# Kernel optimization log

Measured on AMD Instinct MI355X. Metric: run time of the kernel, lower is better.

Reference implementation:

```python
import jax, jax.numpy as jnp
import numpy as np

B, S, NODE, DEP, R, L, E = 32, 1024, 256, 64, 50, 16, 128


def setup_inputs() -> dict:
    key = jax.random.key(0)
    k1, k2, k3, k4, k5 = jax.random.split(key, 5)
    context = jax.random.normal(k1, (B, S, NODE), dtype=jnp.float32)
    # torch.rand -> uniform [0,1); one [dep, node+dep] matrix per dependency relation
    dep_W = jax.random.uniform(k2, (R, DEP, NODE + DEP), dtype=jnp.float32)
    heads = jax.random.randint(k3, (B, L, E), 0, S, dtype=jnp.int32)
    tails = jax.random.randint(k4, (B, L, E), 0, S, dtype=jnp.int32)
    rels = jax.random.randint(k5, (B, L, E), 0, R, dtype=jnp.int32)
    return {"context": context, "dep_W": dep_W, "heads": heads, "tails": tails, "rels": rels}


def reference(context, dep_W, heads, tails, rels):
    # context: [B,S,node]; dep_W: [R,dep,node+dep]; heads/tails/rels: [B,L,E]
    B_, S_, node = context.shape
    dep = dep_W.shape[1]
    E_ = heads.shape[2]
    batch_off = jnp.arange(B_, dtype=jnp.int32)[:, None] * S_  # [B,1]

    def layer_step(child, layer):
        h, t, r = layer  # each [B,E]
        # gather per-edge tail features (node feature ++ child state from deeper layers)
        ctx_t = jnp.take_along_axis(context, t[:, :, None], axis=1)  # [B,E,node]
        chd_t = jnp.take_along_axis(child, t[:, :, None], axis=1)    # [B,E,dep]
        feat = jnp.concatenate([ctx_t, chd_t], axis=-1)              # [B,E,node+dep]
        W_e = dep_W[r]                                               # [B,E,dep,node+dep]
        # sum(W * feat, dim=1) == relation-indexed matvec
        msg = jnp.einsum('bekd,bed->bek', W_e, feat)                 # [B,E,dep]
        # scatter-average messages onto head nodes (per batch -> flat index)
        idx = (batch_off + h).reshape(-1)                            # [B*E]
        seg = jax.ops.segment_sum(msg.reshape(-1, dep), idx, num_segments=B_ * S_)
        cnt = jax.ops.segment_sum(jnp.ones((B_ * E_,), msg.dtype), idx, num_segments=B_ * S_)
        avg = seg / jnp.maximum(cnt, 1.0)[:, None]
        child_flat = child.reshape(B_ * S_, dep)
        # heads touched this layer get the averaged message (assignment semantics)
        child_new = jnp.where((cnt > 0)[:, None], avg, child_flat).reshape(B_, S_, dep)
        return child_new, None

    child0 = jnp.zeros((B_, S_, dep), context.dtype)
    layers = (jnp.moveaxis(heads, 1, 0), jnp.moveaxis(tails, 1, 0), jnp.moveaxis(rels, 1, 0))
    child, _ = jax.lax.scan(layer_step, child0, layers)  # layer 0 = deepest layer
    return jnp.concatenate([context, child], axis=-1)    # [B,S,node+dep]
```

## Files before the change

### kernel.cpp

```cpp
#include <hip/hip_runtime.h>

constexpr int B_ = 32;
constexpr int S_ = 1024;
constexpr int NODE_ = 256;
constexpr int DEP_ = 64;
constexpr int R_ = 50;
constexpr int L_ = 16;
constexpr int E_ = 128;
constexpr int FEAT_ = NODE_ + DEP_;
constexpr int NEDGE_ = B_ * E_;
constexpr int BS_ = B_ * S_;
constexpr int CH_ = 16;
constexpr int NCH_ = 320;
constexpr int PREB_ = 512;
constexpr int GCH_ = 64;
constexpr int NGC_ = 1088;

constexpr size_t N_CHILD  = (size_t)BS_ * DEP_;
constexpr size_t OFF_A0   = N_CHILD;
constexpr size_t OFF_WT   = N_CHILD * 4;
constexpr size_t N_WT     = (size_t)R_ * FEAT_ * DEP_;
constexpr size_t OFF_SORT = OFF_WT + N_WT;
constexpr size_t N_SORT   = (size_t)L_ * NEDGE_;
constexpr size_t OFF_CHUNK= OFF_SORT + N_SORT;
constexpr size_t N_CHUNK_I= (size_t)L_ * NCH_ * 4;
constexpr size_t OFF_HC   = OFF_CHUNK + N_CHUNK_I;
constexpr size_t N_HC     = (size_t)L_ * BS_;
constexpr size_t OFF_MT   = OFF_HC + N_HC;
constexpr size_t OFF_MH   = OFF_MT + N_SORT;
constexpr size_t OFF_MI   = OFF_MH + N_SORT;
constexpr size_t OFF_CD   = OFF_MI + N_SORT;
constexpr size_t N_CD     = (size_t)L_ * NEDGE_ * DEP_;
constexpr size_t OFF_GIDX = OFF_CD + N_CD;
constexpr size_t OFF_GCH  = OFF_GIDX + N_SORT;
constexpr size_t OFF_HLR  = OFF_GCH + (size_t)NGC_ * 4;
constexpr size_t OFF_SLR  = OFF_HLR + (size_t)L_ * R_;

__global__ void k_pre(const float* __restrict__ W, const int* __restrict__ rels,
                      const int* __restrict__ heads,
                      float* __restrict__ WT2, int* __restrict__ sorted,
                      int4* __restrict__ chunks, int* __restrict__ hc,
                      float* __restrict__ zero_base,
                      int* __restrict__ hist_lr, int* __restrict__ start_lr) {
  int blk = blockIdx.x, tid = threadIdx.x;
  if (blk < L_) {
    int l = blk;
    __shared__ int hist[R_], startA[R_], rank[R_], cstart[R_];
    __shared__ int ntot;
    if (tid < R_) { hist[tid] = 0; rank[tid] = 0; }
    int* hcl = hc + (size_t)l * BS_;
    for (int i = tid; i < BS_; i += 256) hcl[i] = 0;
    __syncthreads();
    for (int ed = tid; ed < NEDGE_; ed += 256) {
      int b = ed >> 7, e = ed & (E_ - 1);
      atomicAdd(&hist[rels[(b * L_ + l) * E_ + e]], 1);
      atomicAdd(&hcl[b * S_ + heads[(b * L_ + l) * E_ + e]], 1);
    }
    __syncthreads();
    if (tid == 0) {
      int s = 0, cs = 0;
      for (int r = 0; r < R_; ++r) {
        startA[r] = s; s += hist[r];
        cstart[r] = cs; cs += (hist[r] + CH_ - 1) / CH_;
      }
      ntot = cs;
    }
    __syncthreads();
    for (int ed = tid; ed < NEDGE_; ed += 256) {
      int b = ed >> 7, e = ed & (E_ - 1);
      int r = rels[(b * L_ + l) * E_ + e];
      int pos = startA[r] + atomicAdd(&rank[r], 1);
      sorted[l * NEDGE_ + pos] = ed;
    }
    if (tid < R_) {
      hist_lr[l * R_ + tid] = hist[tid];
      start_lr[l * R_ + tid] = startA[tid];
      int n = hist[tid], st = startA[tid], cs = cstart[tid];
      for (int m = 0; m * CH_ < n; ++m) {
        int c = n - m * CH_; if (c > CH_) c = CH_;
        chunks[l * NCH_ + cs + m] = make_int4(tid, st + m * CH_, c, 0);
      }
    }
    __syncthreads();
    for (int i = ntot + tid; i < NCH_; i += 256)
      chunks[l * NCH_ + i] = make_int4(0, 0, 0, 0);
  } else {
    int gtid = (blk - L_) * 256 + tid;
    const int NT = PREB_ * 256;
    for (int gid = gtid; gid < (int)N_WT; gid += NT) {
      int r = gid / 20480;
      int rem = gid - r * 20480;
      int i4 = rem >> 8;
      int k = (rem >> 2) & 63;
      int c = rem & 3;
      WT2[gid] = W[((size_t)r * DEP_ + k) * FEAT_ + 4 * i4 + c];
    }
    float4* z4 = (float4*)zero_base;
    int nz4 = (int)((N_CHILD * 2) / 4);
    for (int i = gtid; i < nz4; i += NT) z4[i] = make_float4(0.f, 0.f, 0.f, 0.f);
  }
}

__global__ void __launch_bounds__(256) k_gidx(
    const int* __restrict__ hist_lr, const int* __restrict__ start_lr,
    int* __restrict__ gidx, int4* __restrict__ gchunks) {
  int bid = blockIdx.x;
  int r = bid / L_, l = bid - r * L_;
  int tid = threadIdx.x;
  __shared__ int sh[L_ * R_];
  __shared__ int base_s, ntot_s;
  for (int i = tid; i < L_ * R_; i += 256) sh[i] = hist_lr[i];
  __syncthreads();
  if (tid == 0) {
    int goff = 0;
    for (int rr = 0; rr < r; ++rr)
      for (int ll = 0; ll < L_; ++ll) goff += sh[ll * R_ + rr];
    for (int ll = 0; ll < l; ++ll) goff += sh[ll * R_ + r];
    base_s = goff;
  }
  __syncthreads();
  int n = sh[l * R_ + r];
  int st = start_lr[l * R_ + r];
  int base = base_s;
  for (int i = tid; i < n; i += 256)
    gidx[base + i] = l * NEDGE_ + st + i;

  if (bid == 0) {
    __shared__ int tot[R_], goffA[R_], cstart[R_];
    if (tid < R_) {
      int t = 0;
      for (int ll = 0; ll < L_; ++ll) t += sh[ll * R_ + tid];
      tot[tid] = t;
    }
    __syncthreads();
    if (tid == 0) {
      int s = 0, cs = 0;
      for (int rr = 0; rr < R_; ++rr) {
        goffA[rr] = s; s += tot[rr];
        cstart[rr] = cs; cs += (tot[rr] + GCH_ - 1) / GCH_;
      }
      ntot_s = cs;
    }
    __syncthreads();
    if (tid < R_) {
      int nn = tot[tid], go = goffA[tid], cs = cstart[tid];
      for (int m = 0; m * GCH_ < nn; ++m) {
        int c = nn - m * GCH_; if (c > GCH_) c = GCH_;
        gchunks[cs + m] = make_int4(tid, go + m * GCH_, c, 0);
      }
    }
    __syncthreads();
    for (int i = ntot_s + tid; i < NGC_; i += 256)
      gchunks[i] = make_int4(0, 0, 0, 0);
  }
}

__device__ __forceinline__ float dot64(const float4* __restrict__ f4,
                                       const float4* __restrict__ w) {
  float a0 = 0.f, a1 = 0.f, a2 = 0.f, a3 = 0.f;
#pragma unroll
  for (int i = 0; i < 16; ++i) {
    float4 f = f4[i];
    a0 = fmaf(w[i].x, f.x, a0);
    a1 = fmaf(w[i].y, f.y, a1);
    a2 = fmaf(w[i].z, f.z, a2);
    a3 = fmaf(w[i].w, f.w, a3);
  }
  return (a0 + a1) + (a2 + a3);
}

__device__ __forceinline__ void fma4(float& a, float4 w, float4 f) {
  a = fmaf(w.x, f.x, a);
  a = fmaf(w.y, f.y, a);
  a = fmaf(w.z, f.z, a);
  a = fmaf(w.w, f.w, a);
}

__global__ void __launch_bounds__(256, 4) k_ctx2(
    const float* __restrict__ context, const float* __restrict__ WT2,
    const int* __restrict__ heads, const int* __restrict__ tails,
    const int* __restrict__ sorted, const int4* __restrict__ gchunks,
    const int* __restrict__ gidx, const int* __restrict__ hc,
    float* __restrict__ ctxdot, int* __restrict__ m_trow,
    int* __restrict__ m_hrow, float* __restrict__ m_invc) {
  int4 ck = gchunks[blockIdx.x];
  int r = ck.x, gstart = ck.y, gcnt = ck.z;
  if (gcnt == 0) return;
  int tid = threadIdx.x;
  int tk = tid & 15, tj = tid >> 4;

  __shared__ float4 Wn_s[16 * 64];
  __shared__ __align__(16) float F_s[GCH_][68];
  __shared__ int   trow_s[GCH_];
  __shared__ float invc_s[GCH_];
  __shared__ int   pos_s[GCH_];

  if (tid < GCH_) {
    int jj = (tid < gcnt) ? tid : (gcnt - 1);
    int pos = gidx[gstart + jj];
    int l = pos >> 12;
    int ed = sorted[pos];
    int b = ed >> 7, e = ed & (E_ - 1);
    int t = tails[(b * L_ + l) * E_ + e];
    int h = heads[(b * L_ + l) * E_ + e];
    int trow = b * S_ + t, hrow = b * S_ + h;
    float invc = 1.0f / (float)hc[(size_t)l * BS_ + hrow];
    trow_s[tid] = trow;
    invc_s[tid] = invc;
    pos_s[tid] = pos;
    if (tid < gcnt) {
      int tch = (l > 0) && (hc[(size_t)(l - 1) * BS_ + trow] > 0);
      m_trow[pos] = trow | (tch ? (int)0x80000000 : 0);
      m_hrow[pos] = hrow;
      m_invc[pos] = invc;
    }
  }
  __syncthreads();

  float acc[4][4] = {};
  const float4* ctx4 = (const float4*)context;
  const float4* W4 = (const float4*)WT2 + (size_t)r * 80 * 64;

  int jrow = tid >> 2;
  int c0 = tid & 3;
  int trowj = trow_s[jrow];

  float4 wreg[4], freg[4];
#pragma unroll
  for (int rep = 0; rep < 4; ++rep) {
    wreg[rep] = W4[256 * rep + tid];
    freg[rep] = ctx4[(size_t)trowj * 64 + (c0 + 4 * rep)];
  }

  for (int dp = 0; dp < 4; ++dp) {
#pragma unroll
    for (int rep = 0; rep < 4; ++rep) {
      Wn_s[256 * rep + tid] = wreg[rep];
      *(float4*)&F_s[jrow][4 * (c0 + 4 * rep)] = freg[rep];
    }
    __syncthreads();

    if (dp < 3) {
#pragma unroll
      for (int rep = 0; rep < 4; ++rep) {
        wreg[rep] = W4[1024 * (dp + 1) + 256 * rep + tid];
        freg[rep] = ctx4[(size_t)trowj * 64 + (dp + 1) * 16 + (c0 + 4 * rep)];
      }
    }

#pragma unroll
    for (int i4 = 0; i4 < 16; ++i4) {
      float4 wv[4], fv[4];
#pragma unroll
      for (int a = 0; a < 4; ++a) wv[a] = Wn_s[i4 * 64 + tk + 16 * a];
#pragma unroll
      for (int bb = 0; bb < 4; ++bb)
        fv[bb] = *(const float4*)&F_s[4 * tj + bb][4 * i4];
#pragma unroll
      for (int a = 0; a < 4; ++a)
#pragma unroll
        for (int bb = 0; bb < 4; ++bb) fma4(acc[a][bb], wv[a], fv[bb]);
    }
    __syncthreads();
  }

#pragma unroll
  for (int bb = 0; bb < 4; ++bb) {
    int j = 4 * tj + bb;
    if (j < gcnt) {
      float iv = invc_s[j];
      float* rowp = ctxdot + (size_t)pos_s[j] * DEP_;
#pragma unroll
      for (int a = 0; a < 4; ++a) rowp[tk + 16 * a] = acc[a][bb] * iv;
    }
  }
}

__global__ void __launch_bounds__(256) k_layer(
    const float* __restrict__ WT2, float* __restrict__ child,
    const int4* __restrict__ chunks, const int* __restrict__ m_trow,
    const int* __restrict__ m_hrow, const float* __restrict__ m_invc,
    const float* __restrict__ ctxdot, int l,
    const float* __restrict__ Aprev, float* __restrict__ Acur,
    float* __restrict__ Anext) {
  int tid = threadIdx.x;
  int4 ck = chunks[l * NCH_ + blockIdx.x];
  int r = ck.x, start = ck.y, ccnt = ck.z;
  __shared__ float feat[CH_][DEP_];

  if (ccnt > 0) {
    int wv = tid >> 6, k = tid & 63;

    const float4* Wp = (const float4*)WT2 + ((size_t)r * 80 + 64) * 64 + k;
    float4 w[16];
#pragma unroll
    for (int i = 0; i < 16; ++i) w[i] = Wp[(size_t)i * 64];

    int jj[4], valid[4], tch[4], trow[4], hrow[4];
    float invc[4];
#pragma unroll
    for (int u = 0; u < 4; ++u) {
      int j = wv + 4 * u;
      valid[u] = (j < ccnt);
      jj[u] = valid[u] ? j : (ccnt - 1);
      int pos = l * NEDGE_ + start + jj[u];
      int tr = m_trow[pos];
      tch[u] = (tr < 0);
      trow[u] = tr & 0x7fffffff;
      hrow[u] = m_hrow[pos];
      invc[u] = m_invc[pos];
    }

    float v[4];
#pragma unroll
    for (int u = 0; u < 4; ++u) {
      const float* p = tch[u] ? Aprev : child;
      v[u] = p[(size_t)trow[u] * DEP_ + k];
    }
#pragma unroll
    for (int u = 0; u < 4; ++u) feat[jj[u]][k] = v[u];
    __syncthreads();

#pragma unroll
    for (int u = 0; u < 4; ++u) {
      float d = dot64((const float4*)&feat[jj[u]][0], w);
      int pos = l * NEDGE_ + start + jj[u];
      float contrib = d * invc[u] + ctxdot[(size_t)pos * DEP_ + k];
      if (valid[u]) atomicAdd(&Acur[(size_t)hrow[u] * DEP_ + k], contrib);
    }
  }

  int gtid = blockIdx.x * 256 + tid;
  const int NT = NCH_ * 256;
  if (l > 0) {
    const float4* Ap4 = (const float4*)Aprev;
    float4* ch4 = (float4*)child;
    const int* mh = m_hrow + (size_t)(l - 1) * NEDGE_;
    for (int idx = gtid; idx < NEDGE_ * 16; idx += NT) {
      int pos = idx >> 4, c4 = idx & 15;
      int hrow = mh[pos];
      ch4[(size_t)hrow * 16 + c4] = Ap4[(size_t)hrow * 16 + c4];
    }
  }
  if (l + 1 < L_) {
    float4* An4 = (float4*)Anext;
    const int* mh = m_hrow + (size_t)(l + 1) * NEDGE_;
    float4 z = make_float4(0.f, 0.f, 0.f, 0.f);
    for (int idx = gtid; idx < NEDGE_ * 16; idx += NT) {
      int pos = idx >> 4, c4 = idx & 15;
      An4[(size_t)mh[pos] * 16 + c4] = z;
    }
  }
}

__global__ void k_out(const float4* __restrict__ ctx4,
                      const float4* __restrict__ chd4,
                      const float4* __restrict__ A04,
                      const int* __restrict__ hc15,
                      float4* __restrict__ out4) {
  constexpr int TOT4 = B_ * S_ * (FEAT_ / 4);
  int i = blockIdx.x * blockDim.x + threadIdx.x;
  if (i >= TOT4) return;
  int row = i / 80;
  int c4 = i - row * 80;
  float4 v;
  if (c4 < 64) {
    v = ctx4[(size_t)row * 64 + c4];
  } else {
    int k4 = c4 - 64;
    v = (hc15[row] > 0) ? A04[(size_t)row * 16 + k4]
                        : chd4[(size_t)row * 16 + k4];
  }
  out4[i] = v;
}

extern "C" void kernel_launch(void* const* d_in, const int* in_sizes, int n_in,
                              void* d_out, int out_size, void* d_ws, size_t ws_size,
                              hipStream_t stream) {
  const float* context = (const float*)d_in[0];
  const float* dep_W   = (const float*)d_in[1];
  const int*   heads   = (const int*)d_in[2];
  const int*   tails   = (const int*)d_in[3];
  const int*   rels    = (const int*)d_in[4];
  float* out = (float*)d_out;

  float* ws = (float*)d_ws;
  float* child  = ws;
  float* A[3] = { ws + OFF_A0, ws + OFF_A0 + N_CHILD, ws + OFF_A0 + 2 * N_CHILD };
  float* WT2    = ws + OFF_WT;
  int*   sorted = (int*)(ws + OFF_SORT);
  int4*  chunks = (int4*)(ws + OFF_CHUNK);
  int*   hc     = (int*)(ws + OFF_HC);
  int*   m_trow = (int*)(ws + OFF_MT);
  int*   m_hrow = (int*)(ws + OFF_MH);
  float* m_invc = ws + OFF_MI;
  float* ctxdot = ws + OFF_CD;
  int*   gidx   = (int*)(ws + OFF_GIDX);
  int4*  gchunks= (int4*)(ws + OFF_GCH);
  int*   hist_lr= (int*)(ws + OFF_HLR);
  int*   start_lr=(int*)(ws + OFF_SLR);

  k_pre<<<L_ + PREB_, 256, 0, stream>>>(dep_W, rels, heads, WT2, sorted,
                                        chunks, hc, child, hist_lr, start_lr);

  k_gidx<<<R_ * L_, 256, 0, stream>>>(hist_lr, start_lr, gidx, gchunks);

  k_ctx2<<<NGC_, 256, 0, stream>>>(context, WT2, heads, tails, sorted,
                                   gchunks, gidx, hc, ctxdot, m_trow, m_hrow,
                                   m_invc);

  for (int l = 0; l < L_; ++l) {
    float* Acur  = A[l % 3];
    float* Aprev = A[(l + 2) % 3];
    float* Anext = A[(l + 1) % 3];
    k_layer<<<NCH_, 256, 0, stream>>>(WT2, child, chunks, m_trow, m_hrow,
                                      m_invc, ctxdot, l, Aprev, Acur, Anext);
  }

  constexpr int TOT4 = B_ * S_ * (FEAT_ / 4);
  k_out<<<(TOT4 + 255) / 256, 256, 0, stream>>>(
      (const float4*)context, (const float4*)child, (const float4*)A[0],
      hc + (size_t)(L_ - 1) * BS_, (float4*)out);
}
```

Measured before the change: 312.1 us.

## Fuse per-layer launches and output into one persistent kernel with grid barrier

Replaces the 16 per-layer k_layer launches and the k_out launch with a single persistent k_chain kernel of 320 blocks that loops over layers and synchronises with a global atomic-counter barrier, then writes the output. It also stores ctxdot in gather-chunk order via a shared-memory transpose for coalesced writes, indexed through a new m_g map. This removes launch overhead and inter-kernel gaps, at the cost of spin-wait barriers, scalar agent-scope atomic loads and stores in place of float4 copies, and reliance on all 320 blocks being co-resident.

After: 870.4 us. +178.9%, slower.

```diff
diff --git a/kernel.cpp b/kernel.cpp
--- a/kernel.cpp
+++ b/kernel.cpp
@@ -35,13 +35,19 @@
 constexpr size_t OFF_GCH  = OFF_GIDX + N_SORT;
 constexpr size_t OFF_HLR  = OFF_GCH + (size_t)NGC_ * 4;
 constexpr size_t OFF_SLR  = OFF_HLR + (size_t)L_ * R_;
+constexpr size_t OFF_MG   = OFF_SLR + (size_t)L_ * R_;
+constexpr size_t OFF_BAR  = OFF_MG + N_SORT;
+
+#define LD_SC(p)    __hip_atomic_load((p), __ATOMIC_RELAXED, __HIP_MEMORY_SCOPE_AGENT)
+#define ST_SC(p, v) __hip_atomic_store((p), (v), __ATOMIC_RELAXED, __HIP_MEMORY_SCOPE_AGENT)
 
 __global__ void k_pre(const float* __restrict__ W, const int* __restrict__ rels,
                       const int* __restrict__ heads,
                       float* __restrict__ WT2, int* __restrict__ sorted,
                       int4* __restrict__ chunks, int* __restrict__ hc,
                       float* __restrict__ zero_base,
-                      int* __restrict__ hist_lr, int* __restrict__ start_lr) {
+                      int* __restrict__ hist_lr, int* __restrict__ start_lr,
+                      int* __restrict__ bar) {
   int blk = blockIdx.x, tid = threadIdx.x;
   if (blk < L_) {
     int l = blk;
@@ -86,6 +92,7 @@
       chunks[l * NCH_ + i] = make_int4(0, 0, 0, 0);
   } else {
     int gtid = (blk - L_) * 256 + tid;
+    if (gtid == 0) bar[0] = 0;
     const int NT = PREB_ * 256;
     for (int gid = gtid; gid < (int)N_WT; gid += NT) {
       int r = gid / 20480;
@@ -182,7 +189,8 @@
     const int* __restrict__ sorted, const int4* __restrict__ gchunks,
     const int* __restrict__ gidx, const int* __restrict__ hc,
     float* __restrict__ ctxdot, int* __restrict__ m_trow,
-    int* __restrict__ m_hrow, float* __restrict__ m_invc) {
+    int* __restrict__ m_hrow, float* __restrict__ m_invc,
+    int* __restrict__ m_g) {
   int4 ck = gchunks[blockIdx.x];
   int r = ck.x, gstart = ck.y, gcnt = ck.z;
   if (gcnt == 0) return;
@@ -193,7 +201,6 @@
   __shared__ __align__(16) float F_s[GCH_][68];
   __shared__ int   trow_s[GCH_];
   __shared__ float invc_s[GCH_];
-  __shared__ int   pos_s[GCH_];
 
   if (tid < GCH_) {
     int jj = (tid < gcnt) ? tid : (gcnt - 1);
@@ -207,12 +214,12 @@
     float invc = 1.0f / (float)hc[(size_t)l * BS_ + hrow];
     trow_s[tid] = trow;
     invc_s[tid] = invc;
-    pos_s[tid] = pos;
     if (tid < gcnt) {
       int tch = (l > 0) && (hc[(size_t)(l - 1) * BS_ + trow] > 0);
       m_trow[pos] = trow | (tch ? (int)0x80000000 : 0);
       m_hrow[pos] = hrow;
       m_invc[pos] = invc;
+      m_g[pos] = gstart + tid;
     }
   }
   __syncthreads();
@@ -264,114 +271,130 @@
     __syncthreads();
   }
 
+  float* Tr = (float*)Wn_s;
 #pragma unroll
   for (int bb = 0; bb < 4; ++bb) {
     int j = 4 * tj + bb;
-    if (j < gcnt) {
-      float iv = invc_s[j];
-      float* rowp = ctxdot + (size_t)pos_s[j] * DEP_;
-#pragma unroll
-      for (int a = 0; a < 4; ++a) rowp[tk + 16 * a] = acc[a][bb] * iv;
-    }
-  }
-}
-
-__global__ void __launch_bounds__(256) k_layer(
+    float iv = invc_s[j];
+#pragma unroll
+    for (int a = 0; a < 4; ++a) Tr[j * 64 + tk + 16 * a] = acc[a][bb] * iv;
+  }
+  __syncthreads();
+  float4* dst = (float4*)(ctxdot + (size_t)gstart * DEP_);
+  const float4* Tr4 = (const float4*)Tr;
+  int n4 = gcnt * 16;
+  for (int t = tid; t < n4; t += 256) dst[t] = Tr4[t];
+}
+
+__global__ void __launch_bounds__(256, 2) k_chain(
     const float* __restrict__ WT2, float* __restrict__ child,
     const int4* __restrict__ chunks, const int* __restrict__ m_trow,
     const int* __restrict__ m_hrow, const float* __restrict__ m_invc,
-    const float* __restrict__ ctxdot, int l,
-    const float* __restrict__ Aprev, float* __restrict__ Acur,
-    float* __restrict__ Anext) {
+    const float* __restrict__ ctxdot, const int* __restrict__ m_g,
+    float* __restrict__ A0, float* __restrict__ A1, float* __restrict__ A2,
+    const float4* __restrict__ ctx4, const int* __restrict__ hc15,
+    float4* __restrict__ out4, int* __restrict__ bar) {
   int tid = threadIdx.x;
-  int4 ck = chunks[l * NCH_ + blockIdx.x];
-  int r = ck.x, start = ck.y, ccnt = ck.z;
   __shared__ float feat[CH_][DEP_];
-
-  if (ccnt > 0) {
-    int wv = tid >> 6, k = tid & 63;
-
-    const float4* Wp = (const float4*)WT2 + ((size_t)r * 80 + 64) * 64 + k;
-    float4 w[16];
-#pragma unroll
-    for (int i = 0; i < 16; ++i) w[i] = Wp[(size_t)i * 64];
-
-    int jj[4], valid[4], tch[4], trow[4], hrow[4];
-    float invc[4];
-#pragma unroll
-    for (int u = 0; u < 4; ++u) {
-      int j = wv + 4 * u;
-      valid[u] = (j < ccnt);
-      jj[u] = valid[u] ? j : (ccnt - 1);
-      int pos = l * NEDGE_ + start + jj[u];
-      int tr = m_trow[pos];
-      tch[u] = (tr < 0);
-      trow[u] = tr & 0x7fffffff;
-      hrow[u] = m_hrow[pos];
-      invc[u] = m_invc[pos];
-    }
-
-    float v[4];
-#pragma unroll
-    for (int u = 0; u < 4; ++u) {
-      const float* p = tch[u] ? Aprev : child;
-      v[u] = p[(size_t)trow[u] * DEP_ + k];
-    }
-#pragma unroll
-    for (int u = 0; u < 4; ++u) feat[jj[u]][k] = v[u];
-    __syncthreads();
-
-#pragma unroll
-    for (int u = 0; u < 4; ++u) {
-      float d = dot64((const float4*)&feat[jj[u]][0], w);
-      int pos = l * NEDGE_ + start + jj[u];
-      float contrib = d * invc[u] + ctxdot[(size_t)pos * DEP_ + k];
-      if (valid[u]) atomicAdd(&Acur[(size_t)hrow[u] * DEP_ + k], contrib);
-    }
-  }
-
-  int gtid = blockIdx.x * 256 + tid;
-  const int NT = NCH_ * 256;
-  if (l > 0) {
-    const float4* Ap4 = (const float4*)Aprev;
-    float4* ch4 = (float4*)child;
-    const int* mh = m_hrow + (size_t)(l - 1) * NEDGE_;
-    for (int idx = gtid; idx < NEDGE_ * 16; idx += NT) {
-      int pos = idx >> 4, c4 = idx & 15;
-      int hrow = mh[pos];
-      ch4[(size_t)hrow * 16 + c4] = Ap4[(size_t)hrow * 16 + c4];
-    }
-  }
-  if (l + 1 < L_) {
-    float4* An4 = (float4*)Anext;
-    const int* mh = m_hrow + (size_t)(l + 1) * NEDGE_;
-    float4 z = make_float4(0.f, 0.f, 0.f, 0.f);
-    for (int idx = gtid; idx < NEDGE_ * 16; idx += NT) {
-      int pos = idx >> 4, c4 = idx & 15;
-      An4[(size_t)mh[pos] * 16 + c4] = z;
-    }
-  }
-}
-
-__global__ void k_out(const float4* __restrict__ ctx4,
-                      const float4* __restrict__ chd4,
-                      const float4* __restrict__ A04,
-                      const int* __restrict__ hc15,
-                      float4* __restrict__ out4) {
+  float* Abuf[3] = {A0, A1, A2};
+
+  for (int l = 0; l < L_; ++l) {
+    float* Acur = Abuf[l % 3];
+    float* Aprev = Abuf[(l + 2) % 3];
+    float* Anext = Abuf[(l + 1) % 3];
+
+    int4 ck = chunks[l * NCH_ + blockIdx.x];
+    int r = ck.x, start = ck.y, ccnt = ck.z;
+
+    if (ccnt > 0) {
+      int wv = tid >> 6, k = tid & 63;
+
+      const float4* Wp = (const float4*)WT2 + ((size_t)r * 80 + 64) * 64 + k;
+      float4 w[16];
+#pragma unroll
+      for (int i = 0; i < 16; ++i) w[i] = Wp[(size_t)i * 64];
+
+      int jj[4], valid[4], tch[4], trow[4], hrow[4], gg[4];
+      float invc[4];
+#pragma unroll
+      for (int u = 0; u < 4; ++u) {
+        int j = wv + 4 * u;
+        valid[u] = (j < ccnt);
+        jj[u] = valid[u] ? j : (ccnt - 1);
+        int pos = l * NEDGE_ + start + jj[u];
+        int tr = m_trow[pos];
+        tch[u] = (tr < 0);
+        trow[u] = tr & 0x7fffffff;
+        hrow[u] = m_hrow[pos];
+        invc[u] = m_invc[pos];
+        gg[u] = m_g[pos];
+      }
+
+      float v[4];
+#pragma unroll
+      for (int u = 0; u < 4; ++u) {
+        const float* p = tch[u] ? Aprev : child;
+        v[u] = LD_SC(&p[(size_t)trow[u] * DEP_ + k]);
+      }
+#pragma unroll
+      for (int u = 0; u < 4; ++u) feat[jj[u]][k] = v[u];
+      __syncthreads();
+
+#pragma unroll
+      for (int u = 0; u < 4; ++u) {
+        float d = dot64((const float4*)&feat[jj[u]][0], w);
+        float contrib = d * invc[u] + ctxdot[(size_t)gg[u] * DEP_ + k];
+        if (valid[u]) atomicAdd(&Acur[(size_t)hrow[u] * DEP_ + k], contrib);
+      }
+      __syncthreads();
+    }
+
+    int gtid = blockIdx.x * 256 + tid;
+    const int NT = NCH_ * 256;
+    if (l > 0) {
+      const int* mh = m_hrow + (size_t)(l - 1) * NEDGE_;
+      for (int idx = gtid; idx < NEDGE_ * DEP_; idx += NT) {
+        int pos = idx >> 6, c = idx & 63;
+        size_t off = (size_t)mh[pos] * DEP_ + c;
+        ST_SC(&child[off], LD_SC(&Aprev[off]));
+      }
+    }
+    if (l + 1 < L_) {
+      const int* mh = m_hrow + (size_t)(l + 1) * NEDGE_;
+      for (int idx = gtid; idx < NEDGE_ * DEP_; idx += NT) {
+        int pos = idx >> 6, c = idx & 63;
+        ST_SC(&Anext[(size_t)mh[pos] * DEP_ + c], 0.0f);
+      }
+    }
+
+    __syncthreads();
+    if (tid == 0) {
+      __hip_atomic_fetch_add(bar, 1, __ATOMIC_RELEASE, __HIP_MEMORY_SCOPE_AGENT);
+      int target = (l + 1) * NCH_;
+      while (__hip_atomic_load(bar, __ATOMIC_ACQUIRE, __HIP_MEMORY_SCOPE_AGENT) < target)
+        __builtin_amdgcn_s_sleep(8);
+    }
+    __syncthreads();
+  }
+
   constexpr int TOT4 = B_ * S_ * (FEAT_ / 4);
-  int i = blockIdx.x * blockDim.x + threadIdx.x;
-  if (i >= TOT4) return;
-  int row = i / 80;
-  int c4 = i - row * 80;
-  float4 v;
-  if (c4 < 64) {
-    v = ctx4[(size_t)row * 64 + c4];
-  } else {
-    int k4 = c4 - 64;
-    v = (hc15[row] > 0) ? A04[(size_t)row * 16 + k4]
-                        : chd4[(size_t)row * 16 + k4];
-  }
-  out4[i] = v;
+  for (int i = blockIdx.x * 256 + tid; i < TOT4; i += NCH_ * 256) {
+    int row = i / 80;
+    int c4 = i - row * 80;
+    float4 v;
+    if (c4 < 64) {
+      v = ctx4[(size_t)row * 64 + c4];
+    } else {
+      int k4 = c4 - 64;
+      const float* src = (hc15[row] > 0) ? A0 : child;
+      size_t off = (size_t)row * DEP_ + 4 * k4;
+      v.x = LD_SC(&src[off + 0]);
+      v.y = LD_SC(&src[off + 1]);
+      v.z = LD_SC(&src[off + 2]);
+      v.w = LD_SC(&src[off + 3]);
+    }
+    out4[i] = v;
+  }
 }
 
 extern "C" void kernel_launch(void* const* d_in, const int* in_sizes, int n_in,
@@ -386,7 +409,9 @@
 
   float* ws = (float*)d_ws;
   float* child  = ws;
-  float* A[3] = { ws + OFF_A0, ws + OFF_A0 + N_CHILD, ws + OFF_A0 + 2 * N_CHILD };
+  float* A0 = ws + OFF_A0;
+  float* A1 = ws + OFF_A0 + N_CHILD;
+  float* A2 = ws + OFF_A0 + 2 * N_CHILD;
   float* WT2    = ws + OFF_WT;
   int*   sorted = (int*)(ws + OFF_SORT);
   int4*  chunks = (int4*)(ws + OFF_CHUNK);
@@ -399,26 +424,22 @@
   int4*  gchunks= (int4*)(ws + OFF_GCH);
   int*   hist_lr= (int*)(ws + OFF_HLR);
   int*   start_lr=(int*)(ws + OFF_SLR);
+  int*   m_g    = (int*)(ws + OFF_MG);
+  int*   bar    = (int*)(ws + OFF_BAR);
 
   k_pre<<<L_ + PREB_, 256, 0, stream>>>(dep_W, rels, heads, WT2, sorted,
-                                        chunks, hc, child, hist_lr, start_lr);
+                                        chunks, hc, child, hist_lr, start_lr,
+                                        bar);
 
   k_gidx<<<R_ * L_, 256, 0, stream>>>(hist_lr, start_lr, gidx, gchunks);
 
   k_ctx2<<<NGC_, 256, 0, stream>>>(context, WT2, heads, tails, sorted,
                                    gchunks, gidx, hc, ctxdot, m_trow, m_hrow,
-                                   m_invc);
-
-  for (int l = 0; l < L_; ++l) {
-    float* Acur  = A[l % 3];
-    float* Aprev = A[(l + 2) % 3];
-    float* Anext = A[(l + 1) % 3];
-    k_layer<<<NCH_, 256, 0, stream>>>(WT2, child, chunks, m_trow, m_hrow,
-                                      m_invc, ctxdot, l, Aprev, Acur, Anext);
-  }
-
-  constexpr int TOT4 = B_ * S_ * (FEAT_ / 4);
-  k_out<<<(TOT4 + 255) / 256, 256, 0, stream>>>(
-      (const float4*)context, (const float4*)child, (const float4*)A[0],
-      hc + (size_t)(L_ - 1) * BS_, (float4*)out);
-}
+                                   m_invc, m_g);
+
+  k_chain<<<NCH_, 256, 0, stream>>>(WT2, child, chunks, m_trow, m_hrow,
+                                    m_invc, ctxdot, m_g, A0, A1, A2,
+                                    (const float4*)context,
+                                    hc + (size_t)(L_ - 1) * BS_,
+                                    (float4*)out, bar);
+}
```
